# Kernel optimization log

Hardware: AMD Instinct MI355X
Metric: run time of the kernel (lower is better)

## Reference

```python
import jax, jax.numpy as jnp
import numpy as np

D = 1024
H = 16
DH = D // H  # 64


def setup_inputs() -> dict:
    key = jax.random.key(0)
    ks = jax.random.split(key, 11)
    B, T = 4, 2048
    s = 1.0 / np.sqrt(D)
    return {
        "q": jax.random.normal(ks[0], (B, T, D), jnp.float32),
        "k": jax.random.normal(ks[1], (B, T, D), jnp.float32),
        "v": jax.random.normal(ks[2], (B, T, D), jnp.float32),
        "Wq": jax.random.normal(ks[3], (D, D), jnp.float32) * s,
        "bq": jnp.zeros((D,), jnp.float32),
        "Wk": jax.random.normal(ks[4], (D, D), jnp.float32) * s,
        "bk": jnp.zeros((D,), jnp.float32),
        "Wv": jax.random.normal(ks[5], (D, D), jnp.float32) * s,
        "bv": jnp.zeros((D,), jnp.float32),
        "gamma": jnp.ones((D,), jnp.float32),
        "beta": jnp.zeros((D,), jnp.float32),
    }


def _layernorm(x, gamma, beta, eps=1e-8):
    # torch LayerNorm variant: unbiased std, eps added to std (not var)
    mean = jnp.mean(x, axis=-1, keepdims=True)
    var = jnp.sum((x - mean) ** 2, axis=-1, keepdims=True) / (x.shape[-1] - 1)
    std = jnp.sqrt(var)
    return gamma * (x - mean) / (std + eps) + beta


def reference(q, k, v, Wq, bq, Wk, bk, Wv, bv, gamma, beta):
    B, T, _ = q.shape
    # projections (D -> D)
    q_ = q @ Wq + bq
    k_ = k @ Wk + bk
    v_ = v @ Wv + bv
    # head split: chunk(dim=2) + cat(dim=0)  ==  (B,T,H,dh) -> (H,B,T,dh)
    qh = q_.reshape(B, T, H, DH).transpose(2, 0, 1, 3)
    kh = k_.reshape(B, T, H, DH).transpose(2, 0, 1, 3)
    vh = v_.reshape(B, T, H, DH).transpose(2, 0, 1, 3)
    scores = jnp.einsum("hbqd,hbkd->hbqk", qh, kh) / jnp.sqrt(
        jnp.asarray(DH, qh.dtype)
    )
    attn = jax.nn.softmax(scores, axis=-1)
    out = jnp.einsum("hbqk,hbkd->hbqd", attn, vh)  # (H,B,T,dh)
    # merge heads: chunk(dim=0) + cat(dim=2)
    out = out.transpose(1, 2, 0, 3).reshape(B, T, D)
    return _layernorm(out + q, gamma, beta)
```

## Files before the change

### kernel.cpp

```cpp
#include <hip/hip_runtime.h>

constexpr int B  = 4;
constexpr int T  = 2048;
constexpr int D  = 1024;
constexpr int H  = 16;
constexpr int DH = 64;
constexpr int BT = B * T;


typedef __attribute__((ext_vector_type(8))) short bf16x8;
typedef __attribute__((ext_vector_type(4))) float f32x4;
typedef __attribute__((ext_vector_type(4))) unsigned short u16x4;
typedef __attribute__((ext_vector_type(4))) unsigned int u32x4;

static __device__ __forceinline__ unsigned short f2bf(float f) {
    unsigned u = __builtin_bit_cast(unsigned, f);
    unsigned r = (u + 0x7fffu + ((u >> 16) & 1u)) >> 16;
    return (unsigned short)r;
}

static __device__ __forceinline__ unsigned cvt_pk_bf16(float lo, float hi) {
    unsigned r;
    asm("v_cvt_pk_bf16_f32 %0, %1, %2" : "=v"(r) : "v"(lo), "v"(hi));
    return r;
}

static __device__ __forceinline__ void pl32swap(unsigned &a, unsigned &b) {
    asm volatile("v_permlane32_swap_b32 %0, %1" : "+v"(a), "+v"(b));
}
static __device__ __forceinline__ void pl16swap(unsigned &a, unsigned &b) {
    asm volatile("v_permlane16_swap_b32 %0, %1" : "+v"(a), "+v"(b));
}

static __device__ __forceinline__ void stage16(const unsigned short* g, unsigned short* l) {
    __builtin_amdgcn_global_load_lds(
        (const __attribute__((address_space(1))) unsigned int*)g,
        (__attribute__((address_space(3))) unsigned int*)l, 16, 0, 0);
}

__global__ __launch_bounds__(256) void transpose_w(
    const float* __restrict__ Wq,
    const float* __restrict__ Wk,
    const float* __restrict__ Wv,
    unsigned short* __restrict__ WT) {
    __shared__ unsigned short tile[32][33];
    const float* src = (blockIdx.y == 0) ? Wq : (blockIdx.y == 1) ? Wk : Wv;
    unsigned short* dst = WT + (size_t)blockIdx.y * D * D;
    int tx = blockIdx.x % (D / 32);
    int ty = blockIdx.x / (D / 32);
    int c  = threadIdx.x & 31;
    int r0 = threadIdx.x >> 5;
#pragma unroll
    for (int i = 0; i < 4; i++) {
        int r = r0 + i * 8;
        tile[r][c] = f2bf(src[(size_t)(ty * 32 + r) * D + tx * 32 + c]);
    }
    __syncthreads();
#pragma unroll
    for (int i = 0; i < 4; i++) {
        int r = r0 + i * 8;
        dst[(size_t)(tx * 32 + r) * D + ty * 32 + c] = tile[c][r];
    }
}

__global__ __launch_bounds__(256) void x_convert(
    const float* __restrict__ X, unsigned short* __restrict__ Xb) {
    size_t i = ((size_t)blockIdx.x * 256 + threadIdx.x) * 4;
    f32x4 xv = *(const f32x4*)(X + i);
    u16x4 o;
#pragma unroll
    for (int j = 0; j < 4; j++) o[j] = f2bf(xv[j]);
    *(u16x4*)(Xb + i) = o;
}

__global__ __launch_bounds__(256, 2) void qkv_gemm(
    const unsigned short* __restrict__ Xb,
    const unsigned short* __restrict__ Wt,
    const float* __restrict__ bias,
    unsigned short* __restrict__ Qp,
    unsigned short* __restrict__ Kp,
    unsigned short* __restrict__ Vt,
    int which) {
    __shared__ __align__(16) unsigned short Als[128 * 64];
    __shared__ __align__(16) unsigned short Bls[128 * 64];

    int bx   = blockIdx.x;
    int nblk = bx & 7;
    int mblk = bx >> 3;
    int tid  = threadIdx.x;
    int wave = tid >> 6, lane = tid & 63;
    int lane15 = lane & 15, quad = lane >> 4;
    int wm = (wave >> 1) * 64;
    int wn = (wave & 1) * 64;

    const size_t m0 = (size_t)mblk * 128;
    const size_t n0 = (size_t)nblk * 128;

    f32x4 acc[4][4] = {};

    for (int kt = 0; kt < D / 64; kt++) {
        int k0 = kt * 64;
#pragma unroll
        for (int i = 0; i < 4; i++) {
            int gl  = i * 256 + tid;
            int row = gl >> 3, c = gl & 7;
            int sg  = c ^ (row & 7);
            stage16(Xb + (m0 + row) * D + k0 + sg * 8,
                    Als + (size_t)(i * 256 + wave * 64) * 8);
            stage16(Wt + (n0 + row) * D + k0 + sg * 8,
                    Bls + (size_t)(i * 256 + wave * 64) * 8);
        }
        __syncthreads();

        bf16x8 af[2][4], bfr[2][4];
#pragma unroll
        for (int h = 0; h < 2; h++) {
#pragma unroll
            for (int i = 0; i < 4; i++) {
                int rowa = wm + i * 16 + lane15;
                int ga   = (h * 4 + quad) ^ (rowa & 7);
                af[h][i] = *(const bf16x8*)(Als + (size_t)rowa * 64 + ga * 8);
                int rowb = wn + i * 16 + lane15;
                int gb   = (h * 4 + quad) ^ (rowb & 7);
                bfr[h][i] = *(const bf16x8*)(Bls + (size_t)rowb * 64 + gb * 8);
            }
        }
#pragma unroll
        for (int h = 0; h < 2; h++)
#pragma unroll
            for (int mi = 0; mi < 4; mi++)
#pragma unroll
                for (int nf = 0; nf < 4; nf++)
                    acc[mi][nf] = __builtin_amdgcn_mfma_f32_16x16x32_bf16(
                        af[h][mi], bfr[h][nf], acc[mi][nf], 0, 0, 0);
        __syncthreads();
    }

    const float scl = (which == 0) ? 0.18033688011112042f : 1.0f;
#pragma unroll
    for (int nf = 0; nf < 4; nf++) {
        int n = nblk * 128 + wn + nf * 16 + lane15;
        float bn = bias[n];
        int h = n >> 6, d = n & 63;
#pragma unroll
        for (int mi = 0; mi < 4; mi++) {
#pragma unroll
            for (int r = 0; r < 4; r++) {
                int m  = mblk * 128 + wm + mi * 16 + quad * 4 + r;
                int b_ = m >> 11;
                int t  = m & (T - 1);
                unsigned short o = f2bf((acc[mi][nf][r] + bn) * scl);
                if (which == 2) {
                    Vt[(size_t)((b_ * H + h) * DH + d) * T + t] = o;
                } else if (which == 0) {
                    Qp[(size_t)((b_ * H + h) * T + t) * DH + d] = o;
                } else {
                    Kp[(size_t)((b_ * H + h) * T + t) * DH + d] = o;
                }
            }
        }
    }
}

__global__ __launch_bounds__(256, 2) void attn_kernel(
    const unsigned short* __restrict__ Qp,
    const unsigned short* __restrict__ Kp,
    const unsigned short* __restrict__ Vt,
    float* __restrict__ AO) {
    __shared__ __align__(16) unsigned short Kls[2][64 * 64];
    __shared__ __align__(16) unsigned short Vls[2][64 * 64];

    constexpr int NT = T / 64;

    int bx = blockIdx.x;
    int sb = (bx & 7) * 128 + (bx >> 3);
    int qt = sb & 15;
    int bh = sb >> 4;

    int tid  = threadIdx.x;
    int wave = tid >> 6, lane = tid & 63;
    int lane15 = lane & 15, quad = lane >> 4;

    const unsigned short* Qb = Qp + (size_t)bh * T * DH;
    const unsigned short* Kb = Kp + (size_t)bh * T * DH;
    const unsigned short* Vb = Vt + (size_t)bh * DH * T;

    int qbase = qt * 128 + wave * 32;
    bf16x8 qa[2][2];
#pragma unroll
    for (int mi = 0; mi < 2; mi++)
#pragma unroll
        for (int hh = 0; hh < 2; hh++)
            qa[mi][hh] = *(const bf16x8*)(
                Qb + (size_t)(qbase + mi * 16 + lane15) * DH + hh * 32 + quad * 8);

    float ps[2] = {0.f, 0.f};
    f32x4 O[2][4] = {};

#pragma unroll
    for (int i = 0; i < 2; i++) {
        int gl = i * 256 + tid;
        int row = gl >> 3, c = gl & 7;
        int sg = c ^ (row & 7);
        stage16(Kb + (size_t)row * DH + sg * 8,
                &Kls[0][(size_t)(i * 256 + wave * 64) * 8]);
        stage16(Vb + (size_t)row * T + sg * 8,
                &Vls[0][(size_t)(i * 256 + wave * 64) * 8]);
    }
    __syncthreads();

    int cur = 0;
    for (int kt = 0; kt < NT; kt++) {
        if (kt + 1 < NT) {
            int nkb = (kt + 1) * 64;
#pragma unroll
            for (int i = 0; i < 2; i++) {
                int gl = i * 256 + tid;
                int row = gl >> 3, c = gl & 7;
                int sg = c ^ (row & 7);
                stage16(Kb + (size_t)(nkb + row) * DH + sg * 8,
                        &Kls[cur ^ 1][(size_t)(i * 256 + wave * 64) * 8]);
                stage16(Vb + (size_t)row * T + nkb + sg * 8,
                        &Vls[cur ^ 1][(size_t)(i * 256 + wave * 64) * 8]);
            }
        }

        bf16x8 kf[4][2];
#pragma unroll
        for (int nf = 0; nf < 4; nf++) {
            int r = nf * 16 + lane15;
#pragma unroll
            for (int hh = 0; hh < 2; hh++) {
                int ch = (hh * 4 + quad) ^ (r & 7);
                kf[nf][hh] = *(const bf16x8*)(&Kls[cur][(size_t)r * 64 + ch * 8]);
            }
        }

        f32x4 st[4][2] = {};
        __builtin_amdgcn_s_setprio(1);
#pragma unroll
        for (int nf = 0; nf < 4; nf++)
#pragma unroll
            for (int mi = 0; mi < 2; mi++) {
                st[nf][mi] = __builtin_amdgcn_mfma_f32_16x16x32_bf16(
                    kf[nf][0], qa[mi][0], st[nf][mi], 0, 0, 0);
                st[nf][mi] = __builtin_amdgcn_mfma_f32_16x16x32_bf16(
                    kf[nf][1], qa[mi][1], st[nf][mi], 0, 0, 0);
            }
        __builtin_amdgcn_s_setprio(0);

        unsigned e[4][2][2];
#pragma unroll
        for (int nf = 0; nf < 4; nf++)
#pragma unroll
            for (int mi = 0; mi < 2; mi++) {
                f32x4 p;
#pragma unroll
                for (int r = 0; r < 4; r++) {
                    p[r] = __builtin_amdgcn_exp2f(st[nf][mi][r]);
                    ps[mi] += p[r];
                }
                e[nf][mi][0] = cvt_pk_bf16(p[0], p[1]);
                e[nf][mi][1] = cvt_pk_bf16(p[2], p[3]);
            }

        bf16x8 vf[4][2];
#pragma unroll
        for (int nf = 0; nf < 4; nf++) {
            int r = nf * 16 + lane15;
#pragma unroll
            for (int hh = 0; hh < 2; hh++) {
                int ch = (hh * 4 + quad) ^ (r & 7);
                vf[nf][hh] = *(const bf16x8*)(&Vls[cur][(size_t)r * 64 + ch * 8]);
            }
        }

        __builtin_amdgcn_s_setprio(1);
#pragma unroll
        for (int mi = 0; mi < 2; mi++) {
#pragma unroll
            for (int ks = 0; ks < 2; ks++) {
                unsigned a0 = e[2 * ks][mi][0], b0 = e[2 * ks + 1][mi][0];
                pl32swap(a0, b0);
                pl16swap(a0, b0);
                unsigned a1 = e[2 * ks][mi][1], b1 = e[2 * ks + 1][mi][1];
                pl32swap(a1, b1);
                pl16swap(a1, b1);
                u32x4 w;
                w[0] = a0; w[1] = a1; w[2] = b0; w[3] = b1;
                bf16x8 pa = __builtin_bit_cast(bf16x8, w);
#pragma unroll
                for (int nf = 0; nf < 4; nf++)
                    O[mi][nf] = __builtin_amdgcn_mfma_f32_16x16x32_bf16(
                        pa, vf[nf][ks], O[mi][nf], 0, 0, 0);
            }
        }
        __builtin_amdgcn_s_setprio(0);

        __syncthreads();
        cur ^= 1;
    }

    float dinv[2][4];
#pragma unroll
    for (int mi = 0; mi < 2; mi++) {
        ps[mi] += __shfl_xor(ps[mi], 16);
        ps[mi] += __shfl_xor(ps[mi], 32);
        float iv = 1.0f / ps[mi];
#pragma unroll
        for (int r = 0; r < 4; r++)
            dinv[mi][r] = __shfl(iv, (lane & 48) + ((lane >> 4) & 3) * 4 + r);
    }

    int hd = bh & 15;
    int b_ = bh >> 4;
#pragma unroll
    for (int mi = 0; mi < 2; mi++) {
#pragma unroll
        for (int r = 0; r < 4; r++) {
            int t = qbase + mi * 16 + quad * 4 + r;
            float* dst = AO + (size_t)(b_ * T + t) * D + hd * DH;
#pragma unroll
            for (int nf = 0; nf < 4; nf++) {
                dst[nf * 16 + lane15] = O[mi][nf][r] * dinv[mi][r];
            }
        }
    }
}

__global__ __launch_bounds__(256) void ln_kernel(
    float* io,
    const float* __restrict__ qin,
    const float* __restrict__ gamma,
    const float* __restrict__ beta) {
    int row = blockIdx.x;
    int tid = threadIdx.x;
    size_t base = (size_t)row * D;
    float x[4];
    float sum = 0.f, ss = 0.f;
#pragma unroll
    for (int i = 0; i < 4; i++) {
        int c = tid + i * 256;
        float xv = io[base + c] + qin[base + c];
        x[i] = xv;
        sum += xv;
        ss += xv * xv;
    }
#pragma unroll
    for (int off = 32; off >= 1; off >>= 1) {
        sum += __shfl_xor(sum, off);
        ss  += __shfl_xor(ss, off);
    }
    __shared__ float s1[4], s2[4];
    int wave = tid >> 6, lane = tid & 63;
    if (lane == 0) { s1[wave] = sum; s2[wave] = ss; }
    __syncthreads();
    sum = s1[0] + s1[1] + s1[2] + s1[3];
    ss  = s2[0] + s2[1] + s2[2] + s2[3];
    float mean = sum * (1.0f / D);
    float var  = (ss - sum * mean) * (1.0f / (D - 1));
    var = fmaxf(var, 0.0f);
    float inv = 1.0f / (sqrtf(var) + 1e-8f);
#pragma unroll
    for (int i = 0; i < 4; i++) {
        int c = tid + i * 256;
        io[base + c] = gamma[c] * (x[i] - mean) * inv + beta[c];
    }
}

extern "C" void kernel_launch(void* const* d_in, const int* in_sizes, int n_in,
                              void* d_out, int out_size, void* d_ws, size_t ws_size,
                              hipStream_t stream) {
    (void)in_sizes; (void)n_in; (void)out_size; (void)ws_size;
    const float* xin[3] = {(const float*)d_in[0], (const float*)d_in[1], (const float*)d_in[2]};
    const float* Wq  = (const float*)d_in[3];
    const float* bs[3] = {(const float*)d_in[4], (const float*)d_in[6], (const float*)d_in[8]};
    const float* Wk  = (const float*)d_in[5];
    const float* Wv  = (const float*)d_in[7];
    const float* gam = (const float*)d_in[9];
    const float* bet = (const float*)d_in[10];
    float* out = (float*)d_out;

    unsigned short* ws = (unsigned short*)d_ws;
    unsigned short* Qp = ws;
    unsigned short* Kp = Qp + (size_t)BT * D;
    unsigned short* Vt = Kp + (size_t)BT * D;
    unsigned short* WT  = (unsigned short*)d_out;
    unsigned short* Xbf = WT + (size_t)3 * D * D;

    transpose_w<<<dim3((D / 32) * (D / 32), 3), 256, 0, stream>>>(Wq, Wk, Wv, WT);
    for (int which = 0; which < 3; which++) {
        x_convert<<<dim3(BT * D / 1024), 256, 0, stream>>>(xin[which], Xbf);
        qkv_gemm<<<dim3((BT / 128) * (D / 128)), 256, 0, stream>>>(
            Xbf, WT + (size_t)which * D * D, bs[which], Qp, Kp, Vt, which);
    }
    attn_kernel<<<dim3(B * H * (T / 128)), 256, 0, stream>>>(Qp, Kp, Vt, out);
    ln_kernel<<<dim3(BT), 256, 0, stream>>>(out, xin[0], gam, bet);
}
```

Baseline: 345.8 us.

## Fuse fp32-to-bf16 conversion into single batched QKV projection GEMM

Removes the separate x_convert kernels and the per-projection GEMM launches. The three projections now run as one grid indexed by blockIdx.y, and each block loads fp32 activations directly and converts them to bf16 into LDS. The V-transpose epilogue writes four consecutive t values per store, and the layernorm kernel switches to float4 loads and stores. The trade-off is that the activation tiles are now loaded synchronously through registers instead of async staging, which may expose global latency in the GEMM main loop.

```diff
diff --git a/kernel.cpp b/kernel.cpp
--- a/kernel.cpp
+++ b/kernel.cpp
@@ -63,26 +63,24 @@
     }
 }
 
-__global__ __launch_bounds__(256) void x_convert(
-    const float* __restrict__ X, unsigned short* __restrict__ Xb) {
-    size_t i = ((size_t)blockIdx.x * 256 + threadIdx.x) * 4;
-    f32x4 xv = *(const f32x4*)(X + i);
-    u16x4 o;
-#pragma unroll
-    for (int j = 0; j < 4; j++) o[j] = f2bf(xv[j]);
-    *(u16x4*)(Xb + i) = o;
-}
-
-__global__ __launch_bounds__(256, 2) void qkv_gemm(
-    const unsigned short* __restrict__ Xb,
-    const unsigned short* __restrict__ Wt,
-    const float* __restrict__ bias,
+__global__ __launch_bounds__(256, 2) void qkv_gemm_fused(
+    const float* __restrict__ Xq,
+    const float* __restrict__ Xk,
+    const float* __restrict__ Xv,
+    const unsigned short* __restrict__ WTall,
+    const float* __restrict__ bq,
+    const float* __restrict__ bk,
+    const float* __restrict__ bv,
     unsigned short* __restrict__ Qp,
     unsigned short* __restrict__ Kp,
-    unsigned short* __restrict__ Vt,
-    int which) {
+    unsigned short* __restrict__ Vt) {
     __shared__ __align__(16) unsigned short Als[128 * 64];
     __shared__ __align__(16) unsigned short Bls[128 * 64];
+
+    const int which = blockIdx.y;
+    const float* X = (which == 0) ? Xq : (which == 1) ? Xk : Xv;
+    const unsigned short* Wt = WTall + (size_t)which * D * D;
+    const float* bias = (which == 0) ? bq : (which == 1) ? bk : bv;
 
     int bx   = blockIdx.x;
     int nblk = bx & 7;
@@ -105,10 +103,28 @@
             int gl  = i * 256 + tid;
             int row = gl >> 3, c = gl & 7;
             int sg  = c ^ (row & 7);
-            stage16(Xb + (m0 + row) * D + k0 + sg * 8,
-                    Als + (size_t)(i * 256 + wave * 64) * 8);
             stage16(Wt + (n0 + row) * D + k0 + sg * 8,
                     Bls + (size_t)(i * 256 + wave * 64) * 8);
+        }
+        f32x4 xa[4][2];
+#pragma unroll
+        for (int j = 0; j < 4; j++) {
+            int id  = j * 256 + tid;
+            int row = id >> 3, c = id & 7;
+            int sg  = c ^ (row & 7);
+            const float* src = X + (m0 + row) * D + k0 + sg * 8;
+            xa[j][0] = *(const f32x4*)(src);
+            xa[j][1] = *(const f32x4*)(src + 4);
+        }
+#pragma unroll
+        for (int j = 0; j < 4; j++) {
+            int id = j * 256 + tid;
+            u32x4 w;
+            w[0] = cvt_pk_bf16(xa[j][0][0], xa[j][0][1]);
+            w[1] = cvt_pk_bf16(xa[j][0][2], xa[j][0][3]);
+            w[2] = cvt_pk_bf16(xa[j][1][0], xa[j][1][1]);
+            w[3] = cvt_pk_bf16(xa[j][1][2], xa[j][1][3]);
+            *(bf16x8*)(Als + (size_t)id * 8) = __builtin_bit_cast(bf16x8, w);
         }
         __syncthreads();
 
@@ -137,25 +153,39 @@
     }
 
     const float scl = (which == 0) ? 0.18033688011112042f : 1.0f;
-#pragma unroll
-    for (int nf = 0; nf < 4; nf++) {
-        int n = nblk * 128 + wn + nf * 16 + lane15;
-        float bn = bias[n];
-        int h = n >> 6, d = n & 63;
-#pragma unroll
-        for (int mi = 0; mi < 4; mi++) {
-#pragma unroll
-            for (int r = 0; r < 4; r++) {
-                int m  = mblk * 128 + wm + mi * 16 + quad * 4 + r;
-                int b_ = m >> 11;
-                int t  = m & (T - 1);
-                unsigned short o = f2bf((acc[mi][nf][r] + bn) * scl);
-                if (which == 2) {
-                    Vt[(size_t)((b_ * H + h) * DH + d) * T + t] = o;
-                } else if (which == 0) {
-                    Qp[(size_t)((b_ * H + h) * T + t) * DH + d] = o;
-                } else {
-                    Kp[(size_t)((b_ * H + h) * T + t) * DH + d] = o;
+    if (which == 2) {
+#pragma unroll
+        for (int nf = 0; nf < 4; nf++) {
+            int n = nblk * 128 + wn + nf * 16 + lane15;
+            float bn = bias[n];
+            int h = n >> 6, d = n & 63;
+#pragma unroll
+            for (int mi = 0; mi < 4; mi++) {
+                int t0 = mblk * 128 + wm + mi * 16 + quad * 4;
+                int b_ = t0 >> 11;
+                int tt = t0 & (T - 1);
+                u16x4 o;
+#pragma unroll
+                for (int r = 0; r < 4; r++) o[r] = f2bf(acc[mi][nf][r] + bn);
+                *(u16x4*)(Vt + (size_t)((b_ * H + h) * DH + d) * T + tt) = o;
+            }
+        }
+    } else {
+        unsigned short* P = (which == 0) ? Qp : Kp;
+#pragma unroll
+        for (int nf = 0; nf < 4; nf++) {
+            int n = nblk * 128 + wn + nf * 16 + lane15;
+            float bn = bias[n];
+            int h = n >> 6, d = n & 63;
+#pragma unroll
+            for (int mi = 0; mi < 4; mi++) {
+#pragma unroll
+                for (int r = 0; r < 4; r++) {
+                    int m  = mblk * 128 + wm + mi * 16 + quad * 4 + r;
+                    int b_ = m >> 11;
+                    int t  = m & (T - 1);
+                    P[(size_t)((b_ * H + h) * T + t) * DH + d] =
+                        f2bf((acc[mi][nf][r] + bn) * scl);
                 }
             }
         }
@@ -335,16 +365,16 @@
     const float* __restrict__ beta) {
     int row = blockIdx.x;
     int tid = threadIdx.x;
-    size_t base = (size_t)row * D;
-    float x[4];
+    size_t base = (size_t)row * D + tid * 4;
+    f32x4 xo = *(const f32x4*)(io + base);
+    f32x4 xq = *(const f32x4*)(qin + base);
+    f32x4 x;
     float sum = 0.f, ss = 0.f;
 #pragma unroll
     for (int i = 0; i < 4; i++) {
-        int c = tid + i * 256;
-        float xv = io[base + c] + qin[base + c];
-        x[i] = xv;
-        sum += xv;
-        ss += xv * xv;
+        x[i] = xo[i] + xq[i];
+        sum += x[i];
+        ss += x[i] * x[i];
     }
 #pragma unroll
     for (int off = 32; off >= 1; off >>= 1) {
@@ -361,11 +391,12 @@
     float var  = (ss - sum * mean) * (1.0f / (D - 1));
     var = fmaxf(var, 0.0f);
     float inv = 1.0f / (sqrtf(var) + 1e-8f);
-#pragma unroll
-    for (int i = 0; i < 4; i++) {
-        int c = tid + i * 256;
-        io[base + c] = gamma[c] * (x[i] - mean) * inv + beta[c];
-    }
+    f32x4 g = *(const f32x4*)(gamma + tid * 4);
+    f32x4 bb = *(const f32x4*)(beta + tid * 4);
+    f32x4 o;
+#pragma unroll
+    for (int i = 0; i < 4; i++) o[i] = g[i] * (x[i] - mean) * inv + bb[i];
+    *(f32x4*)(io + base) = o;
 }
 
 extern "C" void kernel_launch(void* const* d_in, const int* in_sizes, int n_in,
@@ -374,9 +405,11 @@
     (void)in_sizes; (void)n_in; (void)out_size; (void)ws_size;
     const float* xin[3] = {(const float*)d_in[0], (const float*)d_in[1], (const float*)d_in[2]};
     const float* Wq  = (const float*)d_in[3];
-    const float* bs[3] = {(const float*)d_in[4], (const float*)d_in[6], (const float*)d_in[8]};
+    const float* bq  = (const float*)d_in[4];
     const float* Wk  = (const float*)d_in[5];
+    const float* bk  = (const float*)d_in[6];
     const float* Wv  = (const float*)d_in[7];
+    const float* bv  = (const float*)d_in[8];
     const float* gam = (const float*)d_in[9];
     const float* bet = (const float*)d_in[10];
     float* out = (float*)d_out;
@@ -385,15 +418,11 @@
     unsigned short* Qp = ws;
     unsigned short* Kp = Qp + (size_t)BT * D;
     unsigned short* Vt = Kp + (size_t)BT * D;
-    unsigned short* WT  = (unsigned short*)d_out;
-    unsigned short* Xbf = WT + (size_t)3 * D * D;
+    unsigned short* WT = (unsigned short*)d_out;
 
     transpose_w<<<dim3((D / 32) * (D / 32), 3), 256, 0, stream>>>(Wq, Wk, Wv, WT);
-    for (int which = 0; which < 3; which++) {
-        x_convert<<<dim3(BT * D / 1024), 256, 0, stream>>>(xin[which], Xbf);
-        qkv_gemm<<<dim3((BT / 128) * (D / 128)), 256, 0, stream>>>(
-            Xbf, WT + (size_t)which * D * D, bs[which], Qp, Kp, Vt, which);
-    }
+    qkv_gemm_fused<<<dim3((BT / 128) * (D / 128), 3), 256, 0, stream>>>(
+        xin[0], xin[1], xin[2], WT, bq, bk, bv, Qp, Kp, Vt);
     attn_kernel<<<dim3(B * H * (T / 128)), 256, 0, stream>>>(Qp, Kp, Vt, out);
     ln_kernel<<<dim3(BT), 256, 0, stream>>>(out, xin[0], gam, bet);
 }
```

New measurement: 337.1 us. 2.5% less time.
